# Optimization experiments

Hardware: AMD Instinct MI355X
Metric: run time of the kernel (lower is better)

## Reference

```python
import jax, jax.numpy as jnp
import numpy as np

INPUT_DIM = 2304
SUBSPACE_DIM = 64
ATOMS = 512
NUM_EXPERTS = 256
K = 4


def leaky_offset_relu(x, negative_slope, offset):
    return jnp.where(x >= offset, x, negative_slope * x)


def setup_inputs() -> dict:
    key = jax.random.key(0)
    k0, k1, k2, k3 = jax.random.split(key, 4)
    x = jax.random.normal(k0, (INPUT_DIM,), dtype=jnp.float32)
    # top-level autoencoder encoder (he_uniform approximated by scaled normal)
    enc_top = jax.random.normal(k1, (NUM_EXPERTS, INPUT_DIM), dtype=jnp.float32) * (1.0 / np.sqrt(INPUT_DIM))
    # per-expert down-projection, row-normalized as in __init__
    W_down = jax.random.normal(k2, (NUM_EXPERTS, SUBSPACE_DIM, INPUT_DIM), dtype=jnp.float32)
    W_down = W_down / jnp.linalg.norm(W_down, axis=-1, keepdims=True)
    # per-expert encoder weights, row-normalized as in __init__
    encoder_weights = jax.random.normal(k3, (NUM_EXPERTS, ATOMS, SUBSPACE_DIM), dtype=jnp.float32)
    encoder_weights = encoder_weights / jnp.linalg.norm(encoder_weights, axis=-1, keepdims=True)
    return {"x": x, "enc_top": enc_top, "W_down": W_down, "encoder_weights": encoder_weights}


def reference(x, enc_top, W_down, encoder_weights):
    offset_top = 1.0 / jnp.sqrt(jnp.float32(INPUT_DIM))
    # --- top-level encode: codes = relu_offset(E @ x), negative_slope=0.0 ---
    codes = leaky_offset_relu(enc_top @ x, 0.0, offset_top)  # [num_experts]
    # --- top-k routing (naive_top_k == top_k on a single row) ---
    top_k_values, top_k_indices = jax.lax.top_k(codes, K)  # [k], [k]
    # --- gather per-expert weights, dispatch, expert compute ---
    sel_W_down = W_down[top_k_indices]            # [k, sub, in]
    sel_enc = encoder_weights[top_k_indices]      # [k, atoms, sub]
    subspace_outputs = jnp.einsum('ksd,d->ks', sel_W_down, x)        # [k, sub]
    expert_codes = jnp.einsum('kas,ks->ka', sel_enc, subspace_outputs)  # [k, atoms]
    expert_codes = leaky_offset_relu(expert_codes, 0.01, offset_top)
    # --- decode: top-level decoder is encoder^T; select columns by indices ---
    top_level_output = jnp.einsum('kd,k->d', enc_top[top_k_indices], top_k_values)  # [in]
    # expert decoders are encoder^T, W_up is W_down^T (weight tying)
    decoded_subspace = jnp.einsum('kas,ka->ks', sel_enc, expert_codes)  # [k, sub]
    reconstructed = jnp.einsum('ksd,ks->d', sel_W_down, decoded_subspace)  # sum over experts -> [in]
    return reconstructed + top_level_output
```

## Files before the change

### kernel.cpp

```cpp
#include <hip/hip_runtime.h>
#include <float.h>

#define INPUT_DIM 2304
#define SUB_DIM 64
#define ATOMS 512
#define NUM_EXPERTS 256
#define TOPK 4
#define NBLK 128

#define OFFSET (1.0f / 48.0f)
#define MAGIC 0x9E3779B9u

__device__ __forceinline__ unsigned int flag_ld(const unsigned int* p) {
    return __hip_atomic_load(p, __ATOMIC_RELAXED, __HIP_MEMORY_SCOPE_AGENT);
}
__device__ __forceinline__ void flag_st(unsigned int* p, unsigned int v) {
    __hip_atomic_store(p, v, __ATOMIC_RELAXED, __HIP_MEMORY_SCOPE_AGENT);
}
__device__ __forceinline__ float gldf(const float* p) {
    return __hip_atomic_load(p, __ATOMIC_RELAXED, __HIP_MEMORY_SCOPE_AGENT);
}
__device__ __forceinline__ void gstf(float* p, float v) {
    __hip_atomic_store(p, v, __ATOMIC_RELAXED, __HIP_MEMORY_SCOPE_AGENT);
}


__global__ void __launch_bounds__(256, 1) moe_fused(
    const float* __restrict__ x,
    const float* __restrict__ enc_top,
    const float* __restrict__ W_down,
    const float* __restrict__ enc_w,
    float* __restrict__ out,
    float* __restrict__ ws)
{
    float* codes = ws;
    float* sub   = ws + 256;
    float* dec   = ws + 512;
    unsigned int* fl    = (unsigned int*)((char*)ws + 8192);
    unsigned int* fcode = fl;
    unsigned int* fsub  = fl + NBLK * 64;
    unsigned int* fexp  = fsub + 64;

    __shared__ float s_red[256];
    __shared__ float s_ec[ATOMS];
    __shared__ float s_decp[16][SUB_DIM];
    __shared__ float s_sub[SUB_DIM];
    __shared__ int   s_idx[TOPK];
    __shared__ float s_val[TOPK];

    const int b    = blockIdx.x;
    const int t    = threadIdx.x;
    const int lane = t & 63;
    const int wave = t >> 6;
    const float4* x4 = (const float4*)x;

    if (b < 64) {
        const int c = b * 4 + wave;
        const float4* row4 = (const float4*)(enc_top + (size_t)c * INPUT_DIM);
        float acc = 0.0f;
        #pragma unroll
        for (int i = 0; i < INPUT_DIM / 256; ++i) {
            float4 w  = row4[lane + 64 * i];
            float4 xv = x4[lane + 64 * i];
            acc += w.x * xv.x + w.y * xv.y + w.z * xv.z + w.w * xv.w;
        }
        #pragma unroll
        for (int o = 32; o > 0; o >>= 1) acc += __shfl_down(acc, o);
        if (lane == 0) gstf(&codes[c], (acc >= OFFSET) ? acc : 0.0f);
        __syncthreads();
        if (t < NBLK) flag_st(&fcode[t * 64 + b], MAGIC);
    }

    if (b >= 40 && b < 64) return;

    if (wave == 0) {
        while (!__all(flag_ld(&fcode[b * 64 + lane]) == MAGIC)) {}
        asm volatile("" ::: "memory");
        flag_st(&fcode[b * 64 + lane], 0u);
        float v[4]; int id[4];
        #pragma unroll
        for (int i = 0; i < 4; ++i) { id[i] = lane + 64 * i; v[i] = gldf(&codes[id[i]]); }
        for (int k = 0; k < TOPK; ++k) {
            float bv = v[0]; int bi = id[0];
            #pragma unroll
            for (int i = 1; i < 4; ++i)
                if (v[i] > bv || (v[i] == bv && id[i] < bi)) { bv = v[i]; bi = id[i]; }
            #pragma unroll
            for (int o = 32; o > 0; o >>= 1) {
                float ov = __shfl_down(bv, o);
                int   oi = __shfl_down(bi, o);
                if (ov > bv || (ov == bv && oi < bi)) { bv = ov; bi = oi; }
            }
            bv = __shfl(bv, 0);
            bi = __shfl(bi, 0);
            if (lane == 0) { s_idx[k] = bi; s_val[k] = bv; }
            #pragma unroll
            for (int i = 0; i < 4; ++i)
                if (id[i] == bi) v[i] = -FLT_MAX;
        }
    }
    __syncthreads();

    if (b >= 64) {
        const int r = (b - 64) * 4 + wave;
        const int E = s_idx[r >> 6];
        const float4* row4 = (const float4*)(W_down + ((size_t)E * SUB_DIM + (r & 63)) * INPUT_DIM);
        float acc = 0.0f;
        #pragma unroll
        for (int i = 0; i < INPUT_DIM / 256; ++i) {
            float4 w  = row4[lane + 64 * i];
            float4 xv = x4[lane + 64 * i];
            acc += w.x * xv.x + w.y * xv.y + w.z * xv.z + w.w * xv.w;
        }
        #pragma unroll
        for (int o = 32; o > 0; o >>= 1) acc += __shfl_down(acc, o);
        if (lane == 0) gstf(&sub[r], acc);
        __syncthreads();
        if (t == 0) flag_st(&fsub[b - 64], MAGIC);
        return;
    }

    if (b < TOPK) {
        const int E = s_idx[b];
        const float* W = enc_w + (size_t)E * ATOMS * SUB_DIM;
        float pf = 0.0f;
        #pragma unroll
        for (int i = 0; i < 8; ++i) {
            float4 w = ((const float4*)W)[(size_t)(t + i * 256) * 4];
            pf += w.x + w.y + w.z + w.w;
        }
        if (wave == 0) {
            while (!__all(lane < 16 ? (flag_ld(&fsub[b * 16 + lane]) == MAGIC) : 1)) {}
            asm volatile("" ::: "memory");
            if (lane < 16) flag_st(&fsub[b * 16 + lane], 0u);
            s_sub[lane] = gldf(&sub[b * SUB_DIM + lane]);
        }
        asm volatile("" :: "v"(pf));
        __syncthreads();
        #pragma unroll
        for (int rr = 0; rr < ATOMS / 256; ++rr) {
            int a = t + rr * 256;
            const float4* row4 = (const float4*)(W + (size_t)a * SUB_DIM);
            float acc = 0.0f;
            #pragma unroll
            for (int i = 0; i < SUB_DIM / 4; ++i) {
                float4 w = row4[i];
                acc += w.x * s_sub[4*i] + w.y * s_sub[4*i+1] + w.z * s_sub[4*i+2] + w.w * s_sub[4*i+3];
            }
            s_ec[a] = (acc >= OFFSET) ? acc : 0.01f * acc;
        }
        __syncthreads();
        {
            const int sg = t & 15, ch = t >> 4;
            float4 a4 = make_float4(0.f, 0.f, 0.f, 0.f);
            for (int a = ch * 32; a < ch * 32 + 32; ++a) {
                float4 w = *(const float4*)(W + (size_t)a * SUB_DIM + sg * 4);
                float  e = s_ec[a];
                a4.x += w.x * e; a4.y += w.y * e; a4.z += w.z * e; a4.w += w.w * e;
            }
            *(float4*)&s_decp[ch][sg * 4] = a4;
        }
        __syncthreads();
        if (t < SUB_DIM) {
            float d = 0.0f;
            #pragma unroll
            for (int c = 0; c < 16; ++c) d += s_decp[c][t];
            gstf(&dec[b * SUB_DIM + t], d);
        }
        __syncthreads();
        if (t < 36) flag_st(&fexp[t * 4 + b], MAGIC);
        return;
    }

    {
        const int rb = b - 4;
        const int d  = rb * 64 + lane;
        const int E  = s_idx[wave];
        float wr[SUB_DIM];
        const float* Wb = W_down + (size_t)E * SUB_DIM * INPUT_DIM + d;
        #pragma unroll
        for (int s = 0; s < SUB_DIM; ++s) wr[s] = Wb[(size_t)s * INPUT_DIM];
        const float et = s_val[wave] * enc_top[(size_t)E * INPUT_DIM + d];
        if (wave == 0) {
            while (!__all(lane < TOPK ? (flag_ld(&fexp[rb * 4 + lane]) == MAGIC) : 1)) {}
            asm volatile("" ::: "memory");
            if (lane < TOPK) flag_st(&fexp[rb * 4 + lane], 0u);
        }
        __syncthreads();
        float dv = gldf(&dec[wave * SUB_DIM + lane]);
        float acc = et;
        #pragma unroll
        for (int s = 0; s < SUB_DIM; ++s)
            acc += wr[s] * __shfl(dv, s);
        s_red[t] = acc;
        __syncthreads();
        if (t < 64)
            out[rb * 64 + t] = s_red[t] + s_red[t + 64] + s_red[t + 128] + s_red[t + 192];
    }
}

extern "C" void kernel_launch(void* const* d_in, const int* in_sizes, int n_in,
                              void* d_out, int out_size, void* d_ws, size_t ws_size,
                              hipStream_t stream) {
    const float* x       = (const float*)d_in[0];
    const float* enc_top = (const float*)d_in[1];
    const float* W_down  = (const float*)d_in[2];
    const float* enc_w   = (const float*)d_in[3];
    float* out = (float*)d_out;
    float* ws  = (float*)d_ws;

    moe_fused<<<dim3(NBLK), dim3(256), 0, stream>>>(x, enc_top, W_down, enc_w, out, ws);
}
```

Before: 19.93 us.

## Replace flag-plus-data handoff with packed 64-bit value/tag atomics

```diff
diff --git a/kernel.cpp b/kernel.cpp
--- a/kernel.cpp
+++ b/kernel.cpp
@@ -11,18 +11,19 @@
 #define OFFSET (1.0f / 48.0f)
 #define MAGIC 0x9E3779B9u
 
-__device__ __forceinline__ unsigned int flag_ld(const unsigned int* p) {
+typedef unsigned long long u64;
+
+__device__ __forceinline__ u64 pair_ld(const u64* p) {
     return __hip_atomic_load(p, __ATOMIC_RELAXED, __HIP_MEMORY_SCOPE_AGENT);
 }
-__device__ __forceinline__ void flag_st(unsigned int* p, unsigned int v) {
+__device__ __forceinline__ void pair_st(u64* p, u64 v) {
     __hip_atomic_store(p, v, __ATOMIC_RELAXED, __HIP_MEMORY_SCOPE_AGENT);
 }
-__device__ __forceinline__ float gldf(const float* p) {
-    return __hip_atomic_load(p, __ATOMIC_RELAXED, __HIP_MEMORY_SCOPE_AGENT);
-}
-__device__ __forceinline__ void gstf(float* p, float v) {
-    __hip_atomic_store(p, v, __ATOMIC_RELAXED, __HIP_MEMORY_SCOPE_AGENT);
-}
+__device__ __forceinline__ u64 pack(float f) {
+    return ((u64)__float_as_uint(f) << 32) | (u64)MAGIC;
+}
+__device__ __forceinline__ bool pvalid(u64 v) { return (unsigned)v == MAGIC; }
+__device__ __forceinline__ float payload(u64 v) { return __uint_as_float((unsigned)(v >> 32)); }
 
 
 __global__ void __launch_bounds__(256, 1) moe_fused(
@@ -31,20 +32,17 @@
     const float* __restrict__ W_down,
     const float* __restrict__ enc_w,
     float* __restrict__ out,
-    float* __restrict__ ws)
+    float* __restrict__ ws_f)
 {
-    float* codes = ws;
-    float* sub   = ws + 256;
-    float* dec   = ws + 512;
-    unsigned int* fl    = (unsigned int*)((char*)ws + 8192);
-    unsigned int* fcode = fl;
-    unsigned int* fsub  = fl + NBLK * 64;
-    unsigned int* fexp  = fsub + 64;
+    u64* pc = (u64*)ws_f;
+    u64* ps = pc + 128 * 256;
+    u64* pd = ps + 4 * 64;
 
     __shared__ float s_red[256];
     __shared__ float s_ec[ATOMS];
     __shared__ float s_decp[16][SUB_DIM];
     __shared__ float s_sub[SUB_DIM];
+    __shared__ float s_dec[SUB_DIM];
     __shared__ int   s_idx[TOPK];
     __shared__ float s_val[TOPK];
 
@@ -54,9 +52,15 @@
     const int wave = t >> 6;
     const float4* x4 = (const float4*)x;
 
+    float4 xr[INPUT_DIM / 256];
+    if (b >= 64) {
+        #pragma unroll
+        for (int i = 0; i < INPUT_DIM / 256; ++i) xr[i] = x4[lane + 64 * i];
+    }
+
     if (b < 64) {
-        const int c = b * 4 + wave;
-        const float4* row4 = (const float4*)(enc_top + (size_t)c * INPUT_DIM);
+        const int row = b * 4 + wave;
+        const float4* row4 = (const float4*)(enc_top + (size_t)row * INPUT_DIM);
         float acc = 0.0f;
         #pragma unroll
         for (int i = 0; i < INPUT_DIM / 256; ++i) {
@@ -66,20 +70,26 @@
         }
         #pragma unroll
         for (int o = 32; o > 0; o >>= 1) acc += __shfl_down(acc, o);
-        if (lane == 0) gstf(&codes[c], (acc >= OFFSET) ? acc : 0.0f);
-        __syncthreads();
-        if (t < NBLK) flag_st(&fcode[t * 64 + b], MAGIC);
+        float c = __shfl(acc, 0);
+        c = (c >= OFFSET) ? c : 0.0f;
+        const u64 pv = pack(c);
+        pair_st(&pc[(size_t)lane * 256 + row], pv);
+        pair_st(&pc[(size_t)(lane + 64) * 256 + row], pv);
     }
 
     if (b >= 40 && b < 64) return;
 
     if (wave == 0) {
-        while (!__all(flag_ld(&fcode[b * 64 + lane]) == MAGIC)) {}
-        asm volatile("" ::: "memory");
-        flag_st(&fcode[b * 64 + lane], 0u);
-        float v[4]; int id[4];
-        #pragma unroll
-        for (int i = 0; i < 4; ++i) { id[i] = lane + 64 * i; v[i] = gldf(&codes[id[i]]); }
+        u64 v0, v1, v2, v3;
+        for (;;) {
+            v0 = pair_ld(&pc[(size_t)b * 256 + lane]);
+            v1 = pair_ld(&pc[(size_t)b * 256 + lane + 64]);
+            v2 = pair_ld(&pc[(size_t)b * 256 + lane + 128]);
+            v3 = pair_ld(&pc[(size_t)b * 256 + lane + 192]);
+            if (__all(pvalid(v0) && pvalid(v1) && pvalid(v2) && pvalid(v3))) break;
+        }
+        float v[4] = { payload(v0), payload(v1), payload(v2), payload(v3) };
+        int   id[4] = { lane, lane + 64, lane + 128, lane + 192 };
         for (int k = 0; k < TOPK; ++k) {
             float bv = v[0]; int bi = id[0];
             #pragma unroll
@@ -98,6 +108,10 @@
             for (int i = 0; i < 4; ++i)
                 if (id[i] == bi) v[i] = -FLT_MAX;
         }
+        pair_st(&pc[(size_t)b * 256 + lane], 0ull);
+        pair_st(&pc[(size_t)b * 256 + lane + 64], 0ull);
+        pair_st(&pc[(size_t)b * 256 + lane + 128], 0ull);
+        pair_st(&pc[(size_t)b * 256 + lane + 192], 0ull);
     }
     __syncthreads();
 
@@ -108,15 +122,12 @@
         float acc = 0.0f;
         #pragma unroll
         for (int i = 0; i < INPUT_DIM / 256; ++i) {
-            float4 w  = row4[lane + 64 * i];
-            float4 xv = x4[lane + 64 * i];
-            acc += w.x * xv.x + w.y * xv.y + w.z * xv.z + w.w * xv.w;
+            float4 w = row4[lane + 64 * i];
+            acc += w.x * xr[i].x + w.y * xr[i].y + w.z * xr[i].z + w.w * xr[i].w;
         }
         #pragma unroll
         for (int o = 32; o > 0; o >>= 1) acc += __shfl_down(acc, o);
-        if (lane == 0) gstf(&sub[r], acc);
-        __syncthreads();
-        if (t == 0) flag_st(&fsub[b - 64], MAGIC);
+        if (lane == 0) pair_st(&ps[r], pack(acc));
         return;
     }
 
@@ -130,10 +141,13 @@
             pf += w.x + w.y + w.z + w.w;
         }
         if (wave == 0) {
-            while (!__all(lane < 16 ? (flag_ld(&fsub[b * 16 + lane]) == MAGIC) : 1)) {}
-            asm volatile("" ::: "memory");
-            if (lane < 16) flag_st(&fsub[b * 16 + lane], 0u);
-            s_sub[lane] = gldf(&sub[b * SUB_DIM + lane]);
+            u64 v;
+            for (;;) {
+                v = pair_ld(&ps[b * SUB_DIM + lane]);
+                if (__all(pvalid(v))) break;
+            }
+            s_sub[lane] = payload(v);
+            pair_st(&ps[b * SUB_DIM + lane], 0ull);
         }
         asm volatile("" :: "v"(pf));
         __syncthreads();
@@ -165,10 +179,17 @@
             float d = 0.0f;
             #pragma unroll
             for (int c = 0; c < 16; ++c) d += s_decp[c][t];
-            gstf(&dec[b * SUB_DIM + t], d);
-        }
-        __syncthreads();
-        if (t < 36) flag_st(&fexp[t * 4 + b], MAGIC);
+            s_dec[t] = d;
+        }
+        __syncthreads();
+        {
+            const u64 pv = pack(s_dec[lane]);
+            #pragma unroll
+            for (int i = 0; i < 9; ++i) {
+                const int r = wave + 4 * i;
+                pair_st(&pd[(size_t)r * 256 + b * SUB_DIM + lane], pv);
+            }
+        }
         return;
     }
 
@@ -181,13 +202,13 @@
         #pragma unroll
         for (int s = 0; s < SUB_DIM; ++s) wr[s] = Wb[(size_t)s * INPUT_DIM];
         const float et = s_val[wave] * enc_top[(size_t)E * INPUT_DIM + d];
-        if (wave == 0) {
-            while (!__all(lane < TOPK ? (flag_ld(&fexp[rb * 4 + lane]) == MAGIC) : 1)) {}
-            asm volatile("" ::: "memory");
-            if (lane < TOPK) flag_st(&fexp[rb * 4 + lane], 0u);
-        }
-        __syncthreads();
-        float dv = gldf(&dec[wave * SUB_DIM + lane]);
+        u64 v;
+        for (;;) {
+            v = pair_ld(&pd[(size_t)rb * 256 + wave * SUB_DIM + lane]);
+            if (__all(pvalid(v))) break;
+        }
+        float dv = payload(v);
+        pair_st(&pd[(size_t)rb * 256 + wave * SUB_DIM + lane], 0ull);
         float acc = et;
         #pragma unroll
         for (int s = 0; s < SUB_DIM; ++s)
```

New measurement: 19.99 us. No clear change (+0.3%).
